# Kernel tuning notes

Measured on AMD Instinct MI355X. Metric: run time of the kernel, lower is better.

## Reference

```python
import jax, jax.numpy as jnp
import numpy as np

N_NODES = 50000
N_EDGES = 800000
N_GRAPHS = 256
IN_DIM, HID = 300, 256
C1, C2, C3 = 16, 64, 256


def setup_inputs() -> dict:
    key = jax.random.key(0)
    ks = jax.random.split(key, 16)
    inp = {
        "x": jax.random.normal(ks[0], (N_NODES, IN_DIM), dtype=jnp.float32),
        "edge_index": jax.random.randint(ks[1], (2, N_EDGES), 0, N_NODES, dtype=jnp.int64),
        "batch": jnp.sort(jax.random.randint(ks[2], (N_NODES,), 0, N_GRAPHS, dtype=jnp.int64)),
    }
    def lin(k, fan_in, fan_out):
        s = 1.0 / np.sqrt(fan_in)
        kw, kb = jax.random.split(k)
        return (jax.random.uniform(kw, (fan_in, fan_out), minval=-s, maxval=s, dtype=jnp.float32),
                jax.random.uniform(kb, (fan_out,), minval=-s, maxval=s, dtype=jnp.float32))
    inp["W1"], inp["b1"] = lin(ks[3], IN_DIM, HID)
    inp["W2"], inp["b2"] = lin(ks[4], HID, HID)
    inp["W3"], inp["b3"] = lin(ks[5], HID, HID)
    inp["Wc1"], inp["bc1"] = lin(ks[6], HID, C1)
    inp["Wc2"], inp["bc2"] = lin(ks[7], HID + C1, C2)
    inp["Wc3"], inp["bc3"] = lin(ks[8], HID + C2, C3)
    return inp


def reference(x, edge_index, batch, W1, b1, W2, b2, W3, b3, Wc1, bc1, Wc2, bc2, Wc3, bc3):
    N = x.shape[0]
    loop = jnp.arange(N, dtype=edge_index.dtype)
    src = jnp.concatenate([edge_index[0], loop])   # source nodes (+ self-loops)
    dst = jnp.concatenate([edge_index[1], loop])   # target nodes (+ self-loops)
    # symmetric GCN normalization: deg^{-1/2}[src] * deg^{-1/2}[dst], deg incl self-loops
    deg = jax.ops.segment_sum(jnp.ones(src.shape, x.dtype), dst, num_segments=N)
    dinv = jnp.where(deg > 0, jax.lax.rsqrt(deg), 0.0)
    norm = dinv[src] * dinv[dst]                   # [E+N]

    def gcn_conv(h, W, b):
        h = h @ W                                  # transform first (PyG order)
        msg = h[src] * norm[:, None]               # gather + scale
        return jax.ops.segment_sum(msg, dst, num_segments=N) + b  # scatter-add

    h = jax.nn.relu(gcn_conv(x, W1, b1))           # dropout = identity (eval)
    h = jax.nn.relu(gcn_conv(h, W2, b2))
    h = gcn_conv(h, W3, b3)

    # global mean pool over graphs
    cnt = jax.ops.segment_sum(jnp.ones((N,), x.dtype), batch, num_segments=N_GRAPHS)
    pooled = jax.ops.segment_sum(h, batch, num_segments=N_GRAPHS) / jnp.maximum(cnt, 1.0)[:, None]

    l1 = pooled @ Wc1 + bc1
    p1 = jax.nn.softmax(l1, axis=1)
    l2 = jnp.concatenate([pooled, p1], axis=1) @ Wc2 + bc2
    p2 = jax.nn.softmax(l2, axis=1)
    l3 = jnp.concatenate([pooled, p2], axis=1) @ Wc3 + bc3
    return (l1, l2, l3)
```

## Files before the change

### kernel.cpp

```cpp
#include <hip/hip_runtime.h>
#include <hip/hip_bf16.h>

#define N_NODES 50000
#define N_EDGES 800000
#define N_GRAPHS 256
#define IN_DIM 300
#define HID 256
#define ROWS_PAD 50048
#define GEMM_GB 391
#define FILL_NB 3125

typedef __bf16 bf16x8 __attribute__((ext_vector_type(8)));
typedef short  s16x8  __attribute__((ext_vector_type(8)));
typedef short  s16x4  __attribute__((ext_vector_type(4)));
typedef float  f32x4  __attribute__((ext_vector_type(4)));
typedef float  f32x2  __attribute__((ext_vector_type(2)));

static __device__ __forceinline__ ushort f2bf(float f) {
    union { float f; uint u; } v; v.f = f;
    uint u = v.u;
    uint r = (u + 0x7fffu + ((u >> 16) & 1u)) >> 16;
    return (ushort)r;
}
static __device__ __forceinline__ float bf2f(ushort b) {
    union { uint u; float f; } v; v.u = ((uint)b) << 16;
    return v.f;
}
static __device__ __forceinline__ unsigned char f2fp8(float f) {
    int pk = __builtin_amdgcn_cvt_pk_fp8_f32(f, f, 0, 0);
    return (unsigned char)(pk & 0xff);
}


__global__ __launch_bounds__(256) void pre_k(const float* __restrict__ W1,
                                             const float* __restrict__ W2,
                                             const float* __restrict__ W3,
                                             ushort* __restrict__ Wt1,
                                             ushort* __restrict__ Wt2,
                                             ushort* __restrict__ Wt3,
                                             const int* __restrict__ dst,
                                             int* __restrict__ cnt) {
    int b = blockIdx.x;
    int n = threadIdx.x;
    if (b < 320) {
        int k = b;
        Wt1[(size_t)n * 320 + k] = (k < IN_DIM) ? f2bf(W1[(size_t)k * 256 + n]) : (ushort)0;
    } else if (b < 576) {
        int k = b - 320;
        Wt2[(size_t)n * 256 + k] = f2bf(W2[(size_t)k * 256 + n]);
    } else if (b < 832) {
        int k = b - 576;
        Wt3[(size_t)n * 256 + k] = f2bf(W3[(size_t)k * 256 + n]);
    } else {
        int e = (b - 832) * 256 + n;
        if (e < N_EDGES) atomicAdd(&cnt[dst[e]], 1);
    }
}


__global__ void scan1(const int* __restrict__ cnt, int* __restrict__ rp,
                      int* __restrict__ bsums, float* __restrict__ dinv, int n) {
    __shared__ int s[256];
    int i = blockIdx.x * 256 + threadIdx.x;
    int v = (i < n) ? cnt[i] : 0;
    if (i < n) dinv[i] = rsqrtf((float)(v + 1));
    s[threadIdx.x] = v;
    __syncthreads();
    for (int off = 1; off < 256; off <<= 1) {
        int t = (threadIdx.x >= off) ? s[threadIdx.x - off] : 0;
        __syncthreads();
        s[threadIdx.x] += t;
        __syncthreads();
    }
    if (i < n) rp[i] = s[threadIdx.x] - v;
    if (threadIdx.x == 255) bsums[blockIdx.x] = s[255];
}

__global__ void scan2(int* __restrict__ bsums, int nb) {
    __shared__ int s[256];
    int v = (threadIdx.x < nb) ? bsums[threadIdx.x] : 0;
    s[threadIdx.x] = v;
    __syncthreads();
    for (int off = 1; off < 256; off <<= 1) {
        int t = (threadIdx.x >= off) ? s[threadIdx.x - off] : 0;
        __syncthreads();
        s[threadIdx.x] += t;
        __syncthreads();
    }
    if (threadIdx.x < nb) bsums[threadIdx.x] = s[threadIdx.x] - v;
}

__global__ void scan3(int* __restrict__ rp, int* __restrict__ cursor,
                      const int* __restrict__ bsums, int n) {
    int i = blockIdx.x * 256 + threadIdx.x;
    if (i < n) {
        int v = rp[i] + bsums[blockIdx.x];
        rp[i] = v;
        cursor[i] = v;
    }
}


template <int KP, int KACT, bool AF32>
static __device__ __forceinline__ void gemm_body(int bx, const void* __restrict__ Ap,
                                                 const ushort* __restrict__ Bt,
                                                 unsigned char* __restrict__ C, int M,
                                                 ushort* As, ushort* Bs) {
    int t = threadIdx.x;
    int wave = t >> 6, lane = t & 63, quad = lane >> 4, l16 = lane & 15;
    int r0 = bx * 128;
    int arow = t & 127;
    int ahalf = t >> 7;

    f32x4 acc[8][4] = {};

    for (int kc = 0; kc < KP; kc += 64) {
#pragma unroll
        for (int i = 0; i < 8; ++i) {
            *(s16x8*)(Bs + i * 2048 + t * 8) =
                *(const s16x8*)(Bt + (size_t)t * KP + kc + i * 8);
        }
#pragma unroll
        for (int i = 0; i < 4; ++i) {
            int ks = 2 * i + ahalf;
            int kg = kc + ks * 8;
            if constexpr (AF32) {
                const float* Af = (const float*)Ap;
                int rg = r0 + arow; if (rg >= M) rg = M - 1;
                ushort tmp[8];
                if (kg + 8 <= KACT) {
                    f32x4 f0 = *(const f32x4*)(Af + (size_t)rg * KACT + kg);
                    f32x4 f1 = *(const f32x4*)(Af + (size_t)rg * KACT + kg + 4);
#pragma unroll
                    for (int j = 0; j < 4; ++j) { tmp[j] = f2bf(f0[j]); tmp[4 + j] = f2bf(f1[j]); }
                } else if (kg < KACT) {
                    f32x4 f0 = *(const f32x4*)(Af + (size_t)rg * KACT + kg);
#pragma unroll
                    for (int j = 0; j < 4; ++j) { tmp[j] = f2bf(f0[j]); tmp[4 + j] = 0; }
                } else {
#pragma unroll
                    for (int j = 0; j < 8; ++j) tmp[j] = 0;
                }
                *(s16x8*)(As + ks * 1024 + arow * 8) = *(const s16x8*)tmp;
            } else {
                const ushort* A = (const ushort*)Ap;
                *(s16x8*)(As + ks * 1024 + arow * 8) =
                    *(const s16x8*)(A + (size_t)(r0 + arow) * KP + kg);
            }
        }
        __syncthreads();

#pragma unroll
        for (int ks = 0; ks < 2; ++ks) {
            bf16x8 b[4];
#pragma unroll
            for (int ct = 0; ct < 4; ++ct)
                b[ct] = __builtin_bit_cast(bf16x8,
                    *(const s16x8*)(Bs + (ks * 4 + quad) * 2048 + (wave * 64 + ct * 16 + l16) * 8));
#pragma unroll
            for (int rt = 0; rt < 8; ++rt) {
                bf16x8 a = __builtin_bit_cast(bf16x8,
                    *(const s16x8*)(As + (ks * 4 + quad) * 1024 + (rt * 16 + l16) * 8));
#pragma unroll
                for (int ct = 0; ct < 4; ++ct)
                    acc[rt][ct] = __builtin_amdgcn_mfma_f32_16x16x32_bf16(a, b[ct], acc[rt][ct], 0, 0, 0);
            }
        }
        __syncthreads();
    }

#pragma unroll
    for (int rt = 0; rt < 8; ++rt) {
        int rowb = r0 + rt * 16 + quad * 4;
#pragma unroll
        for (int ct = 0; ct < 4; ++ct) {
            int col = wave * 64 + ct * 16 + l16;
#pragma unroll
            for (int i = 0; i < 4; ++i)
                C[(size_t)(rowb + i) * 256 + col] = f2fp8(acc[rt][ct][i]);
        }
    }
}

template <int KP, int KACT, bool AF32>
__global__ __launch_bounds__(256, 2) void gemm_k(const void* __restrict__ Ap,
                                                 const ushort* __restrict__ Bt,
                                                 unsigned char* __restrict__ C, int M) {
    __shared__ __align__(16) ushort As[8 * 128 * 8];
    __shared__ __align__(16) ushort Bs[8 * 256 * 8];
    gemm_body<KP, KACT, AF32>(blockIdx.x, Ap, Bt, C, M, As, Bs);
}

__global__ __launch_bounds__(256, 2) void gemm1_fill(const float* __restrict__ x,
                                                     const ushort* __restrict__ Wt1,
                                                     unsigned char* __restrict__ C, int M,
                                                     const int* __restrict__ src,
                                                     const int* __restrict__ dst,
                                                     int* __restrict__ cursor,
                                                     int* __restrict__ col) {
    __shared__ __align__(16) ushort As[8 * 128 * 8];
    __shared__ __align__(16) ushort Bs[8 * 256 * 8];
    int b = blockIdx.x;
    if (b < GEMM_GB) {
        gemm_body<320, IN_DIM, true>(b, x, Wt1, C, M, As, Bs);
    } else {
        int e = (b - GEMM_GB) * 256 + threadIdx.x;
        if (e < N_EDGES) {
            int d = dst[e];
            int p = atomicAdd(&cursor[d], 1);
            col[p] = src[e];
        }
    }
}


__global__ __launch_bounds__(256) void aggregate_fp8(const unsigned char* __restrict__ z,
                                                     ushort* __restrict__ out,
                                                     const int* __restrict__ rp,
                                                     const int* __restrict__ cnt,
                                                     const int* __restrict__ col,
                                                     const float* __restrict__ dinv,
                                                     const float* __restrict__ bias, int relu) {
    const uint* zu = (const uint*)z;
    int t = threadIdx.x;
    int wave = __builtin_amdgcn_readfirstlane(t >> 6);
    int lane = t & 63;
    int n = blockIdx.x * 4 + wave;
    int start = rp[n];
    int c = cnt[n];
    float dv = dinv[n];

    float a0 = 0.f, a1 = 0.f, a2 = 0.f, a3 = 0.f;

    int j = 0;
    for (; j + 4 <= c; j += 4) {
        int r0 = col[start + j], r1 = col[start + j + 1];
        int r2 = col[start + j + 2], r3 = col[start + j + 3];
        float w0 = dinv[r0], w1 = dinv[r1], w2 = dinv[r2], w3 = dinv[r3];
        uint v0 = zu[(size_t)r0 * 64 + lane];
        uint v1 = zu[(size_t)r1 * 64 + lane];
        uint v2 = zu[(size_t)r2 * 64 + lane];
        uint v3 = zu[(size_t)r3 * 64 + lane];
        f32x2 p, q;
        p = __builtin_amdgcn_cvt_pk_f32_fp8(v0, 0); q = __builtin_amdgcn_cvt_pk_f32_fp8(v0, 1);
        a0 += w0 * p[0]; a1 += w0 * p[1]; a2 += w0 * q[0]; a3 += w0 * q[1];
        p = __builtin_amdgcn_cvt_pk_f32_fp8(v1, 0); q = __builtin_amdgcn_cvt_pk_f32_fp8(v1, 1);
        a0 += w1 * p[0]; a1 += w1 * p[1]; a2 += w1 * q[0]; a3 += w1 * q[1];
        p = __builtin_amdgcn_cvt_pk_f32_fp8(v2, 0); q = __builtin_amdgcn_cvt_pk_f32_fp8(v2, 1);
        a0 += w2 * p[0]; a1 += w2 * p[1]; a2 += w2 * q[0]; a3 += w2 * q[1];
        p = __builtin_amdgcn_cvt_pk_f32_fp8(v3, 0); q = __builtin_amdgcn_cvt_pk_f32_fp8(v3, 1);
        a0 += w3 * p[0]; a1 += w3 * p[1]; a2 += w3 * q[0]; a3 += w3 * q[1];
    }
    for (; j < c; ++j) {
        int r = col[start + j];
        float w = dinv[r];
        uint v = zu[(size_t)r * 64 + lane];
        f32x2 p = __builtin_amdgcn_cvt_pk_f32_fp8(v, 0);
        f32x2 q = __builtin_amdgcn_cvt_pk_f32_fp8(v, 1);
        a0 += w * p[0]; a1 += w * p[1]; a2 += w * q[0]; a3 += w * q[1];
    }

    uint vs = zu[(size_t)n * 64 + lane];
    f32x2 sp = __builtin_amdgcn_cvt_pk_f32_fp8(vs, 0);
    f32x2 sq = __builtin_amdgcn_cvt_pk_f32_fp8(vs, 1);
    float sv[4] = {sp[0], sp[1], sq[0], sq[1]};
    f32x4 bv = *(const f32x4*)(bias + lane * 4);
    ushort o[4];
#pragma unroll
    for (int i = 0; i < 4; ++i) {
        float acc = (i == 0 ? a0 : i == 1 ? a1 : i == 2 ? a2 : a3);
        float r = dv * (acc + dv * sv[i]) + bv[i];
        if (relu) r = fmaxf(r, 0.f);
        o[i] = f2bf(r);
    }
    *(s16x4*)(out + (size_t)n * HID + (size_t)lane * 4) = *(const s16x4*)o;
}


__global__ __launch_bounds__(256) void pool_sum(const ushort* __restrict__ h,
                                                const int* __restrict__ batch,
                                                float* __restrict__ psum, int n) {
    int f = threadIdx.x;
    int r0 = blockIdx.x * 64;
    int rend = min(r0 + 64, n);
    if (r0 >= n) return;
    int g = batch[r0];
    float acc = 0.f;
    for (int r = r0; r < rend; ++r) {
        int gr = batch[r];
        if (gr != g) {
            atomicAdd(&psum[g * HID + f], acc);
            acc = 0.f;
            g = gr;
        }
        acc += bf2f(h[(size_t)r * HID + f]);
    }
    atomicAdd(&psum[g * HID + f], acc);
}


__global__ __launch_bounds__(256) void head_k(const float* __restrict__ psum,
                                              const int* __restrict__ batch, int n,
                                              const float* __restrict__ Wc1, const float* __restrict__ bc1,
                                              const float* __restrict__ Wc2, const float* __restrict__ bc2,
                                              const float* __restrict__ Wc3, const float* __restrict__ bc3,
                                              float* __restrict__ out) {
    int g = blockIdx.x;
    int t = threadIdx.x;
    __shared__ float pr[256];
    __shared__ float l1s[16], p1s[16];
    __shared__ float l2s[64], p2s[64];
    int lo = 0, hi = n;
    while (lo < hi) { int mid = (lo + hi) >> 1; if (batch[mid] < g) lo = mid + 1; else hi = mid; }
    int start = lo;
    lo = start; hi = n;
    while (lo < hi) { int mid = (lo + hi) >> 1; if (batch[mid] < g + 1) lo = mid + 1; else hi = mid; }
    int c = lo - start;
    float inv_c = 1.f / (float)max(c, 1);
    pr[t] = psum[g * 256 + t] * inv_c;
    __syncthreads();
    if (t < 16) {
        float a = bc1[t];
        for (int k = 0; k < 256; ++k) a += pr[k] * Wc1[k * 16 + t];
        l1s[t] = a;
        out[g * 16 + t] = a;
    }
    __syncthreads();
    if (t == 0) {
        float m = -1e30f;
        for (int j = 0; j < 16; ++j) m = fmaxf(m, l1s[j]);
        float s = 0.f;
        for (int j = 0; j < 16; ++j) { float e = expf(l1s[j] - m); p1s[j] = e; s += e; }
        float inv = 1.f / s;
        for (int j = 0; j < 16; ++j) p1s[j] *= inv;
    }
    __syncthreads();
    if (t < 64) {
        float a = bc2[t];
        for (int k = 0; k < 256; ++k) a += pr[k] * Wc2[k * 64 + t];
        for (int k = 0; k < 16; ++k) a += p1s[k] * Wc2[(256 + k) * 64 + t];
        l2s[t] = a;
        out[4096 + g * 64 + t] = a;
    }
    __syncthreads();
    if (t == 0) {
        float m = -1e30f;
        for (int j = 0; j < 64; ++j) m = fmaxf(m, l2s[j]);
        float s = 0.f;
        for (int j = 0; j < 64; ++j) { float e = expf(l2s[j] - m); p2s[j] = e; s += e; }
        float inv = 1.f / s;
        for (int j = 0; j < 64; ++j) p2s[j] *= inv;
    }
    __syncthreads();
    {
        float a = bc3[t];
        for (int k = 0; k < 256; ++k) a += pr[k] * Wc3[k * 256 + t];
        for (int k = 0; k < 64; ++k) a += p2s[k] * Wc3[(256 + k) * 256 + t];
        out[4096 + 16384 + g * 256 + t] = a;
    }
}


extern "C" void kernel_launch(void* const* d_in, const int* in_sizes, int n_in,
                              void* d_out, int out_size, void* d_ws, size_t ws_size,
                              hipStream_t stream) {
    const float* x    = (const float*)d_in[0];
    const int*   ei   = (const int*)d_in[1];
    const int*   batch= (const int*)d_in[2];
    const float* W1 = (const float*)d_in[3];  const float* b1 = (const float*)d_in[4];
    const float* W2 = (const float*)d_in[5];  const float* b2 = (const float*)d_in[6];
    const float* W3 = (const float*)d_in[7];  const float* b3 = (const float*)d_in[8];
    const float* Wc1= (const float*)d_in[9];  const float* bc1= (const float*)d_in[10];
    const float* Wc2= (const float*)d_in[11]; const float* bc2= (const float*)d_in[12];
    const float* Wc3= (const float*)d_in[13]; const float* bc3= (const float*)d_in[14];
    float* out = (float*)d_out;

    const int N = N_NODES, E = N_EDGES, G = N_GRAPHS;

    char* ws = (char*)d_ws;
    size_t off = 0;
    auto alloc = [&](size_t bytes) -> void* {
        void* p = ws + off;
        off = (off + bytes + 255) & ~(size_t)255;
        return p;
    };
    unsigned char* z = (unsigned char*)alloc((size_t)ROWS_PAD * HID);
    ushort* hb   = (ushort*)alloc((size_t)ROWS_PAD * HID * 2);
    ushort* Wt1  = (ushort*)alloc((size_t)256 * 320 * 2);
    ushort* Wt2  = (ushort*)alloc((size_t)256 * 256 * 2);
    ushort* Wt3  = (ushort*)alloc((size_t)256 * 256 * 2);
    int*   cnt    = (int*)alloc((size_t)N * 4);
    int*   rp     = (int*)alloc((size_t)N * 4);
    int*   cursor = (int*)alloc((size_t)N * 4);
    float* dinv   = (float*)alloc((size_t)N * 4);
    int*   col    = (int*)alloc((size_t)E * 4);
    float* psum   = (float*)alloc((size_t)G * HID * 4);
    int*   bsums  = (int*)alloc(256 * 4);
    (void)ws_size;

    const int* src = ei;
    const int* dst = ei + E;

    hipMemsetAsync(cnt, 0, (size_t)N * 4, stream);
    hipMemsetAsync(psum, 0, (size_t)G * HID * 4, stream);

    pre_k<<<832 + FILL_NB, 256, 0, stream>>>(W1, W2, W3, Wt1, Wt2, Wt3, dst, cnt);

    const int NB = (N + 255) / 256;
    scan1<<<NB, 256, 0, stream>>>(cnt, rp, bsums, dinv, N);
    scan2<<<1, 256, 0, stream>>>(bsums, NB);
    scan3<<<NB, 256, 0, stream>>>(rp, cursor, bsums, N);

    gemm1_fill<<<GEMM_GB + FILL_NB, 256, 0, stream>>>(x, Wt1, z, N, src, dst, cursor, col);

    aggregate_fp8<<<N / 4, 256, 0, stream>>>(z, hb, rp, cnt, col, dinv, b1, 1);
    gemm_k<256, 256, false><<<GEMM_GB, 256, 0, stream>>>(hb, Wt2, z, N);
    aggregate_fp8<<<N / 4, 256, 0, stream>>>(z, hb, rp, cnt, col, dinv, b2, 1);
    gemm_k<256, 256, false><<<GEMM_GB, 256, 0, stream>>>(hb, Wt3, z, N);
    aggregate_fp8<<<N / 4, 256, 0, stream>>>(z, hb, rp, cnt, col, dinv, b3, 0);

    pool_sum<<<ROWS_PAD / 64, 256, 0, stream>>>(hb, batch, psum, N);
    head_k<<<G, 256, 0, stream>>>(psum, batch, N, Wc1, bc1, Wc2, bc2, Wc3, bc3, out);
}
```

Baseline: 425.6 us.

## Split GEMM tiles into 128x128 with 2x2 wave layout; vectorize edge atomics

```diff
diff --git a/kernel.cpp b/kernel.cpp
--- a/kernel.cpp
+++ b/kernel.cpp
@@ -7,14 +7,16 @@
 #define IN_DIM 300
 #define HID 256
 #define ROWS_PAD 50048
-#define GEMM_GB 391
-#define FILL_NB 3125
+#define GB2 782
+#define EPB 1024
+#define FILLB 782
 
 typedef __bf16 bf16x8 __attribute__((ext_vector_type(8)));
 typedef short  s16x8  __attribute__((ext_vector_type(8)));
 typedef short  s16x4  __attribute__((ext_vector_type(4)));
 typedef float  f32x4  __attribute__((ext_vector_type(4)));
 typedef float  f32x2  __attribute__((ext_vector_type(2)));
+typedef int    i32x4  __attribute__((ext_vector_type(4)));
 
 static __device__ __forceinline__ ushort f2bf(float f) {
     union { float f; uint u; } v; v.f = f;
@@ -52,8 +54,17 @@
         int k = b - 576;
         Wt3[(size_t)n * 256 + k] = f2bf(W3[(size_t)k * 256 + n]);
     } else {
-        int e = (b - 832) * 256 + n;
-        if (e < N_EDGES) atomicAdd(&cnt[dst[e]], 1);
+        int e0 = (b - 832) * EPB + n * 4;
+        if (e0 + 4 <= N_EDGES) {
+            i32x4 d = *(const i32x4*)(dst + e0);
+            atomicAdd(&cnt[d[0]], 1);
+            atomicAdd(&cnt[d[1]], 1);
+            atomicAdd(&cnt[d[2]], 1);
+            atomicAdd(&cnt[d[3]], 1);
+        } else {
+            for (int j = 0; j < 4; ++j)
+                if (e0 + j < N_EDGES) atomicAdd(&cnt[dst[e0 + j]], 1);
+        }
     }
 }
 
@@ -108,25 +119,28 @@
                                                  ushort* As, ushort* Bs) {
     int t = threadIdx.x;
     int wave = t >> 6, lane = t & 63, quad = lane >> 4, l16 = lane & 15;
-    int r0 = bx * 128;
-    int arow = t & 127;
-    int ahalf = t >> 7;
-
-    f32x4 acc[8][4] = {};
+    int wm = wave >> 1, wn = wave & 1;
+    int r0 = (bx >> 1) * 128;
+    int n0 = (bx & 1) * 128;
+    int srow = t & 127;
+    int shalf = t >> 7;
+
+    f32x4 acc[4][4] = {};
 
     for (int kc = 0; kc < KP; kc += 64) {
 #pragma unroll
-        for (int i = 0; i < 8; ++i) {
-            *(s16x8*)(Bs + i * 2048 + t * 8) =
-                *(const s16x8*)(Bt + (size_t)t * KP + kc + i * 8);
-        }
-#pragma unroll
         for (int i = 0; i < 4; ++i) {
-            int ks = 2 * i + ahalf;
+            int ks = 2 * i + shalf;
+            *(s16x8*)(Bs + ks * 1024 + srow * 8) =
+                *(const s16x8*)(Bt + (size_t)(n0 + srow) * KP + kc + ks * 8);
+        }
+#pragma unroll
+        for (int i = 0; i < 4; ++i) {
+            int ks = 2 * i + shalf;
             int kg = kc + ks * 8;
             if constexpr (AF32) {
                 const float* Af = (const float*)Ap;
-                int rg = r0 + arow; if (rg >= M) rg = M - 1;
+                int rg = r0 + srow; if (rg >= M) rg = M - 1;
                 ushort tmp[8];
                 if (kg + 8 <= KACT) {
                     f32x4 f0 = *(const f32x4*)(Af + (size_t)rg * KACT + kg);
@@ -141,40 +155,41 @@
 #pragma unroll
                     for (int j = 0; j < 8; ++j) tmp[j] = 0;
                 }
-                *(s16x8*)(As + ks * 1024 + arow * 8) = *(const s16x8*)tmp;
+                *(s16x8*)(As + ks * 1024 + srow * 8) = *(const s16x8*)tmp;
             } else {
                 const ushort* A = (const ushort*)Ap;
-                *(s16x8*)(As + ks * 1024 + arow * 8) =
-                    *(const s16x8*)(A + (size_t)(r0 + arow) * KP + kg);
+                *(s16x8*)(As + ks * 1024 + srow * 8) =
+                    *(const s16x8*)(A + (size_t)(r0 + srow) * KP + kg);
             }
         }
         __syncthreads();
 
 #pragma unroll
-        for (int ks = 0; ks < 2; ++ks) {
-            bf16x8 b[4];
+        for (int ks2 = 0; ks2 < 2; ++ks2) {
+            bf16x8 a[4], b[4];
 #pragma unroll
             for (int ct = 0; ct < 4; ++ct)
                 b[ct] = __builtin_bit_cast(bf16x8,
-                    *(const s16x8*)(Bs + (ks * 4 + quad) * 2048 + (wave * 64 + ct * 16 + l16) * 8));
-#pragma unroll
-            for (int rt = 0; rt < 8; ++rt) {
-                bf16x8 a = __builtin_bit_cast(bf16x8,
-                    *(const s16x8*)(As + (ks * 4 + quad) * 1024 + (rt * 16 + l16) * 8));
+                    *(const s16x8*)(Bs + (ks2 * 4 + quad) * 1024 + (wn * 64 + ct * 16 + l16) * 8));
+#pragma unroll
+            for (int rt = 0; rt < 4; ++rt)
+                a[rt] = __builtin_bit_cast(bf16x8,
+                    *(const s16x8*)(As + (ks2 * 4 + quad) * 1024 + (wm * 64 + rt * 16 + l16) * 8));
+#pragma unroll
+            for (int rt = 0; rt < 4; ++rt)
 #pragma unroll
                 for (int ct = 0; ct < 4; ++ct)
-                    acc[rt][ct] = __builtin_amdgcn_mfma_f32_16x16x32_bf16(a, b[ct], acc[rt][ct], 0, 0, 0);
-            }
-        }
-        __syncthreads();
-    }
-
-#pragma unroll
-    for (int rt = 0; rt < 8; ++rt) {
-        int rowb = r0 + rt * 16 + quad * 4;
+                    acc[rt][ct] = __builtin_amdgcn_mfma_f32_16x16x32_bf16(a[rt], b[ct], acc[rt][ct], 0, 0, 0);
+        }
+        __syncthreads();
+    }
+
+#pragma unroll
+    for (int rt = 0; rt < 4; ++rt) {
+        int rowb = r0 + wm * 64 + rt * 16 + quad * 4;
 #pragma unroll
         for (int ct = 0; ct < 4; ++ct) {
-            int col = wave * 64 + ct * 16 + l16;
+            int col = n0 + wn * 64 + ct * 16 + l16;
 #pragma unroll
             for (int i = 0; i < 4; ++i)
                 C[(size_t)(rowb + i) * 256 + col] = f2fp8(acc[rt][ct][i]);
@@ -183,15 +198,15 @@
 }
 
 template <int KP, int KACT, bool AF32>
-__global__ __launch_bounds__(256, 2) void gemm_k(const void* __restrict__ Ap,
+__global__ __launch_bounds__(256, 4) void gemm_k(const void* __restrict__ Ap,
                                                  const ushort* __restrict__ Bt,
                                                  unsigned char* __restrict__ C, int M) {
     __shared__ __align__(16) ushort As[8 * 128 * 8];
-    __shared__ __align__(16) ushort Bs[8 * 256 * 8];
+    __shared__ __align__(16) ushort Bs[8 * 128 * 8];
     gemm_body<KP, KACT, AF32>(blockIdx.x, Ap, Bt, C, M, As, Bs);
 }
 
-__global__ __launch_bounds__(256, 2) void gemm1_fill(const float* __restrict__ x,
+__global__ __launch_bounds__(256, 3) void gemm1_fill(const float* __restrict__ x,
                                                      const ushort* __restrict__ Wt1,
                                                      unsigned char* __restrict__ C, int M,
                                                      const int* __restrict__ src,
@@ -199,16 +214,28 @@
                                                      int* __restrict__ cursor,
                                                      int* __restrict__ col) {
     __shared__ __align__(16) ushort As[8 * 128 * 8];
-    __shared__ __align__(16) ushort Bs[8 * 256 * 8];
+    __shared__ __align__(16) ushort Bs[8 * 128 * 8];
     int b = blockIdx.x;
-    if (b < GEMM_GB) {
+    if (b < GB2) {
         gemm_body<320, IN_DIM, true>(b, x, Wt1, C, M, As, Bs);
     } else {
-        int e = (b - GEMM_GB) * 256 + threadIdx.x;
-        if (e < N_EDGES) {
-            int d = dst[e];
-            int p = atomicAdd(&cursor[d], 1);
-            col[p] = src[e];
+        int e0 = (b - GB2) * EPB + threadIdx.x * 4;
+        if (e0 + 4 <= N_EDGES) {
+            i32x4 d = *(const i32x4*)(dst + e0);
+            i32x4 s = *(const i32x4*)(src + e0);
+            int p0 = atomicAdd(&cursor[d[0]], 1);
+            int p1 = atomicAdd(&cursor[d[1]], 1);
+            int p2 = atomicAdd(&cursor[d[2]], 1);
+            int p3 = atomicAdd(&cursor[d[3]], 1);
+            col[p0] = s[0]; col[p1] = s[1]; col[p2] = s[2]; col[p3] = s[3];
+        } else {
+            for (int j = 0; j < 4; ++j) {
+                int e = e0 + j;
+                if (e < N_EDGES) {
+                    int p = atomicAdd(&cursor[dst[e]], 1);
+                    col[p] = src[e];
+                }
+            }
         }
     }
 }
@@ -404,19 +431,19 @@
     hipMemsetAsync(cnt, 0, (size_t)N * 4, stream);
     hipMemsetAsync(psum, 0, (size_t)G * HID * 4, stream);
 
-    pre_k<<<832 + FILL_NB, 256, 0, stream>>>(W1, W2, W3, Wt1, Wt2, Wt3, dst, cnt);
+    pre_k<<<832 + FILLB, 256, 0, stream>>>(W1, W2, W3, Wt1, Wt2, Wt3, dst, cnt);
 
     const int NB = (N + 255) / 256;
     scan1<<<NB, 256, 0, stream>>>(cnt, rp, bsums, dinv, N);
     scan2<<<1, 256, 0, stream>>>(bsums, NB);
     scan3<<<NB, 256, 0, stream>>>(rp, cursor, bsums, N);
 
-    gemm1_fill<<<GEMM_GB + FILL_NB, 256, 0, stream>>>(x, Wt1, z, N, src, dst, cursor, col);
+    gemm1_fill<<<GB2 + FILLB, 256, 0, stream>>>(x, Wt1, z, N, src, dst, cursor, col);
 
     aggregate_fp8<<<N / 4, 256, 0, stream>>>(z, hb, rp, cnt, col, dinv, b1, 1);
-    gemm_k<256, 256, false><<<GEMM_GB, 256, 0, stream>>>(hb, Wt2, z, N);
+    gemm_k<256, 256, false><<<GB2, 256, 0, stream>>>(hb, Wt2, z, N);
     aggregate_fp8<<<N / 4, 256, 0, stream>>>(z, hb, rp, cnt, col, dinv, b2, 1);
-    gemm_k<256, 256, false><<<GEMM_GB, 256, 0, stream>>>(hb, Wt3, z, N);
+    gemm_k<256, 256, false><<<GB2, 256, 0, stream>>>(hb, Wt3, z, N);
     aggregate_fp8<<<N / 4, 256, 0, stream>>>(z, hb, rp, cnt, col, dinv, b3, 0);
 
     pool_sum<<<ROWS_PAD / 64, 256, 0, stream>>>(hb, batch, psum, N);
```

New measurement: 432.7 us. No clear change (+1.7%).
